# Performance work log

Hardware: AMD Instinct MI355X
Metric: run time of the kernel (lower is better)

Reference implementation:

```python
import jax, jax.numpy as jnp
import numpy as np

LN_EPS = 1e-5


def setup_inputs() -> dict:
    key = jax.random.key(0)
    ks = jax.random.split(key, 12)
    b, m, d = 4096, 64, 256
    s = 1.0 / np.sqrt(d)
    return {
        "head_left": jax.random.normal(ks[0], (b, d), jnp.float32),
        "rel_left": jax.random.normal(ks[1], (b, m, d), jnp.float32),
        "tail_left": jax.random.normal(ks[2], (b, m, d), jnp.float32),
        "head_right": jax.random.normal(ks[3], (b, d), jnp.float32),
        "rel_right": jax.random.normal(ks[4], (b, m, d), jnp.float32),
        "tail_right": jax.random.normal(ks[5], (b, m, d), jnp.float32),
        "mask_left": jax.random.randint(ks[6], (b, m), 0, 2).astype(bool),
        "mask_right": jax.random.randint(ks[7], (b, m), 0, 2).astype(bool),
        "bilinear_w": jax.random.normal(ks[8], (d, d), jnp.float32) * s,
        "w_tail": jax.random.normal(ks[9], (d, d), jnp.float32) * s,
        "w_head": jax.random.normal(ks[10], (d, d), jnp.float32) * s,
        "ln_gamma": jnp.ones((d,), jnp.float32),
        "ln_beta": jnp.zeros((d,), jnp.float32),
    }


def _intra_attention(weak_rel, rel, tail, mask, bilinear_w):
    # score[b,m] = weak_rel[b,:] @ W @ rel[b,m,:]  (nn.Bilinear with out=1, no bias)
    hW = weak_rel @ bilinear_w                      # [b, d]
    score = jnp.einsum("bd,bmd->bm", hW, rel)       # [b, m]
    score = jnp.where(mask, -jnp.inf, score)
    att = jax.nn.softmax(score, axis=1)             # [b, m]
    return jnp.einsum("bm,bmd->bd", att, tail)      # weighted sum of tails


def _layer_norm(x, gamma, beta):
    mu = jnp.mean(x, axis=-1, keepdims=True)
    var = jnp.var(x, axis=-1, keepdims=True)
    return (x - mu) * jax.lax.rsqrt(var + LN_EPS) * gamma + beta


def reference(head_left, rel_left, tail_left, head_right, rel_right, tail_right,
              mask_left, mask_right, bilinear_w, w_tail, w_head, ln_gamma, ln_beta):
    weak_rel = head_right - head_left
    left = _intra_attention(weak_rel, rel_left, tail_left, mask_left, bilinear_w)
    right = _intra_attention(weak_rel, rel_right, tail_right, mask_right, bilinear_w)
    # torch Linear: x @ W.T ; dropout p=0.0 is identity
    left = jax.nn.relu(left @ w_tail.T + head_left @ w_head.T)
    right = jax.nn.relu(right @ w_tail.T + head_right @ w_head.T)
    left = _layer_norm(left + head_left, ln_gamma, ln_beta)
    right = _layer_norm(right + head_right, ln_gamma, ln_beta)
    return (left, right)
```

## Files before the change

### kernel.cpp

```cpp
#include <hip/hip_runtime.h>

#define NB 4096
#define MM 64
#define DD 256
#define LN_EPS 1e-5f
#define NEG_BIG -1e30f

typedef float f4v __attribute__((ext_vector_type(4)));

#define WS_WCAT 0
#define WS_HW   (512 * DD)
#define WS_CTX  (WS_HW + NB * DD)

__global__ __launch_bounds__(256)
void k_prep(const float* __restrict__ head_left,
            const float* __restrict__ head_right,
            const float* __restrict__ bw,
            const float* __restrict__ wt,
            const float* __restrict__ wh,
            float* __restrict__ wcat,
            float* __restrict__ hW)
{
    __shared__ float smem[64 * 65];
    const int t = threadIdx.x;

    if (blockIdx.x < 32) {
        const int mat   = blockIdx.x >> 4;
        const int tile  = blockIdx.x & 15;
        const int dBase = (tile >> 2) * 64;
        const int kBase = (tile & 3) * 64;
        const float* __restrict__ w = mat ? wh : wt;
        float (*tile_s)[65] = (float(*)[65])smem;
        const int c  = t & 63;
        const int rr = t >> 6;
        #pragma unroll
        for (int r = rr; r < 64; r += 4)
            tile_s[r][c] = w[(dBase + r) * DD + kBase + c];
        __syncthreads();
        #pragma unroll
        for (int kr = rr; kr < 64; kr += 4)
            wcat[(mat * 256 + kBase + kr) * DD + dBase + c] = tile_s[c][kr];
    } else {
        const int blk  = blockIdx.x - 32;
        const int lane = t & 63;
        const int w    = t >> 6;
        float (*weak_s)[DD] = (float(*)[DD])smem;
        #pragma unroll
        for (int r = 0; r < 16; ++r) {
            const size_t idx = (size_t)(blk * 16 + r) * DD + t;
            weak_s[r][t] = head_right[idx] - head_left[idx];
        }
        __syncthreads();

        float4 acc[4];
        #pragma unroll
        for (int r = 0; r < 4; ++r) acc[r] = make_float4(0.f, 0.f, 0.f, 0.f);
        for (int k = 0; k < DD; ++k) {
            const float4 w4 = *(const float4*)(bw + k * DD + 4 * lane);
            #pragma unroll
            for (int r = 0; r < 4; ++r) {
                const float x = weak_s[4 * w + r][k];
                acc[r].x += x * w4.x; acc[r].y += x * w4.y;
                acc[r].z += x * w4.z; acc[r].w += x * w4.w;
            }
        }
        #pragma unroll
        for (int r = 0; r < 4; ++r)
            *(float4*)(hW + (size_t)(blk * 16 + 4 * w + r) * DD + 4 * lane) = acc[r];
    }
}

__global__ __launch_bounds__(256)
void k_attn(const float* __restrict__ rel_left,
            const float* __restrict__ tail_left,
            const float* __restrict__ rel_right,
            const float* __restrict__ tail_right,
            const unsigned char* __restrict__ mask_left,
            const unsigned char* __restrict__ mask_right,
            const float* __restrict__ hW,
            float* __restrict__ ctx)
{
    const int b    = blockIdx.x >> 1;
    const int side = blockIdx.x & 1;
    const int t    = threadIdx.x;
    const int lane = t & 63;
    const int w    = t >> 6;

    const float* __restrict__ rel  = side ? rel_right  : rel_left;
    const float* __restrict__ tail = side ? tail_right : tail_left;
    const unsigned char* __restrict__ mask = side ? mask_right : mask_left;

    __shared__ float part_s[MM][65];
    __shared__ float red_s[MM][5];
    __shared__ float att_s[MM];
    __shared__ float cpart_s[4][DD];

    const float4 hw4 = *(const float4*)(hW + (size_t)b * DD + 4 * lane);
    const float* rp = rel  + (size_t)b * MM * DD + 4 * lane;
    const float* tp = tail + (size_t)b * MM * DD + 4 * lane;

    #pragma unroll
    for (int i = 0; i < 16; ++i) {
        const int m = w * 16 + i;
        const f4v r4 = __builtin_nontemporal_load((const f4v*)(rp + (size_t)m * DD));
        part_s[m][lane] = hw4.x * r4.x + hw4.y * r4.y + hw4.z * r4.z + hw4.w * r4.w;
    }
    __syncthreads();

    {
        const int m = t & 63;
        const int c = t >> 6;
        float s = 0.f;
        #pragma unroll
        for (int j = 0; j < 16; ++j) s += part_s[m][c * 16 + j];
        red_s[m][c] = s;
    }
    __syncthreads();

    if (w == 0) {
        const unsigned char v0 = mask_left[lane];
        const bool mask_u8 = (__ballot(((lane & 3) != 0) && (v0 != 0)) != 0ULL);

        float s = red_s[lane][0] + red_s[lane][1] + red_s[lane][2] + red_s[lane][3];
        const bool msk = mask_u8
            ? (mask[(size_t)b * MM + lane] != 0)
            : (((const int*)(const void*)mask)[(size_t)b * MM + lane] != 0);
        if (msk) s = NEG_BIG;
        float mx = s;
        #pragma unroll
        for (int off = 32; off >= 1; off >>= 1) mx = fmaxf(mx, __shfl_xor(mx, off, 64));
        const float e = __expf(s - mx);
        float sum = e;
        #pragma unroll
        for (int off = 32; off >= 1; off >>= 1) sum += __shfl_xor(sum, off, 64);
        att_s[lane] = e / sum;
    }
    __syncthreads();

    float4 acc = make_float4(0.f, 0.f, 0.f, 0.f);
    #pragma unroll 4
    for (int i = 0; i < 16; ++i) {
        const int m = w * 16 + i;
        const float a  = att_s[m];
        const f4v v = __builtin_nontemporal_load((const f4v*)(tp + (size_t)m * DD));
        acc.x += a * v.x; acc.y += a * v.y; acc.z += a * v.z; acc.w += a * v.w;
    }
    *(float4*)(&cpart_s[w][4 * lane]) = acc;
    __syncthreads();

    const float sum = cpart_s[0][t] + cpart_s[1][t] + cpart_s[2][t] + cpart_s[3][t];
    ctx[(size_t)(side * NB + b) * DD + t] = sum;
}

__global__ __launch_bounds__(256)
void k_outln(const float* __restrict__ ctx,
             const float* __restrict__ head_left,
             const float* __restrict__ head_right,
             const float* __restrict__ wcat,
             const float* __restrict__ gamma,
             const float* __restrict__ beta,
             float* __restrict__ out)
{
    const int blk  = blockIdx.x;
    const int t    = threadIdx.x;
    const int lane = t & 63;
    const int w    = t >> 6;

    __shared__ float x_s[16][512];

    const int  side = (blk * 16) >> 12;
    const float* __restrict__ head = side ? head_right : head_left;

    #pragma unroll
    for (int i = 0; i < 32; ++i) {
        const int idx = i * 256 + t;
        const int r   = idx >> 9;
        const int c   = idx & 511;
        const int rg  = blk * 16 + r;
        const int bb  = rg & (NB - 1);
        x_s[r][c] = (c < DD) ? ctx[(size_t)rg * DD + c]
                             : head[(size_t)bb * DD + (c - DD)];
    }
    __syncthreads();

    float4 acc[4];
    #pragma unroll
    for (int r = 0; r < 4; ++r) acc[r] = make_float4(0.f, 0.f, 0.f, 0.f);

    #pragma unroll 4
    for (int k = 0; k < 512; ++k) {
        const float4 w4 = *(const float4*)(wcat + (size_t)k * DD + 4 * lane);
        #pragma unroll
        for (int r = 0; r < 4; ++r) {
            const float x = x_s[4 * w + r][k];
            acc[r].x += x * w4.x; acc[r].y += x * w4.y;
            acc[r].z += x * w4.z; acc[r].w += x * w4.w;
        }
    }

    const float4 g4 = *(const float4*)(gamma + 4 * lane);
    const float4 b4 = *(const float4*)(beta  + 4 * lane);

    #pragma unroll
    for (int r = 0; r < 4; ++r) {
        const int rl = 4 * w + r;
        const float4 h4 = *(const float4*)(&x_s[rl][DD + 4 * lane]);
        float4 y;
        y.x = fmaxf(acc[r].x, 0.f) + h4.x;
        y.y = fmaxf(acc[r].y, 0.f) + h4.y;
        y.z = fmaxf(acc[r].z, 0.f) + h4.z;
        y.w = fmaxf(acc[r].w, 0.f) + h4.w;

        float s1 = y.x + y.y + y.z + y.w;
        float s2 = y.x * y.x + y.y * y.y + y.z * y.z + y.w * y.w;
        #pragma unroll
        for (int off = 32; off >= 1; off >>= 1) {
            s1 += __shfl_xor(s1, off, 64);
            s2 += __shfl_xor(s2, off, 64);
        }
        const float mu   = s1 * (1.0f / DD);
        const float var  = s2 * (1.0f / DD) - mu * mu;
        const float rstd = rsqrtf(var + LN_EPS);

        float4 o;
        o.x = (y.x - mu) * rstd * g4.x + b4.x;
        o.y = (y.y - mu) * rstd * g4.y + b4.y;
        o.z = (y.z - mu) * rstd * g4.z + b4.z;
        o.w = (y.w - mu) * rstd * g4.w + b4.w;
        *(float4*)(out + (size_t)(blk * 16 + rl) * DD + 4 * lane) = o;
    }
}

extern "C" void kernel_launch(void* const* d_in, const int* in_sizes, int n_in,
                              void* d_out, int out_size, void* d_ws, size_t ws_size,
                              hipStream_t stream) {
    const float* head_left  = (const float*)d_in[0];
    const float* rel_left   = (const float*)d_in[1];
    const float* tail_left  = (const float*)d_in[2];
    const float* head_right = (const float*)d_in[3];
    const float* rel_right  = (const float*)d_in[4];
    const float* tail_right = (const float*)d_in[5];
    const unsigned char* mask_left  = (const unsigned char*)d_in[6];
    const unsigned char* mask_right = (const unsigned char*)d_in[7];
    const float* bw    = (const float*)d_in[8];
    const float* wt    = (const float*)d_in[9];
    const float* wh    = (const float*)d_in[10];
    const float* gamma = (const float*)d_in[11];
    const float* beta  = (const float*)d_in[12];
    float* out = (float*)d_out;

    float* ws   = (float*)d_ws;
    float* wcat = ws + WS_WCAT;
    float* hW   = ws + WS_HW;
    float* ctxb = ws + WS_CTX;

    k_prep <<<dim3(288),  dim3(256), 0, stream>>>(head_left, head_right, bw, wt, wh, wcat, hW);
    k_attn <<<dim3(8192), dim3(256), 0, stream>>>(rel_left, tail_left, rel_right, tail_right,
                                                  mask_left, mask_right, hW, ctxb);
    k_outln<<<dim3(512),  dim3(256), 0, stream>>>(ctxb, head_left, head_right, wcat,
                                                  gamma, beta, out);
}
```

Measured before the change: 249.8 us.

## Drop LDS staging in output GEMM; each wave computes 8 rows from global

The output projection and LayerNorm kernel no longer stages 16 rows of ctx and head into shared memory. Each wave now handles 8 rows and reads its activations straight from global memory through wave-uniform addresses, which should turn into scalar loads. The block count is halved, so every weight float4 load is reused across 8 rows instead of 4. Outputs are written with nontemporal stores. In exchange there are fewer blocks (256 on a large GPU), more accumulator registers per thread, and a dependence on scalar-cache reads of the activations.

```diff
diff --git a/kernel.cpp b/kernel.cpp
--- a/kernel.cpp
+++ b/kernel.cpp
@@ -166,35 +166,39 @@
     const int lane = t & 63;
     const int w    = t >> 6;
 
-    __shared__ float x_s[16][512];
-
-    const int  side = (blk * 16) >> 12;
+    const int rg0  = __builtin_amdgcn_readfirstlane(blk * 32 + w * 8);
+    const int side = rg0 >> 12;
+    const int bb0  = rg0 & (NB - 1);
     const float* __restrict__ head = side ? head_right : head_left;
 
+    float4 acc[8];
     #pragma unroll
-    for (int i = 0; i < 32; ++i) {
-        const int idx = i * 256 + t;
-        const int r   = idx >> 9;
-        const int c   = idx & 511;
-        const int rg  = blk * 16 + r;
-        const int bb  = rg & (NB - 1);
-        x_s[r][c] = (c < DD) ? ctx[(size_t)rg * DD + c]
-                             : head[(size_t)bb * DD + (c - DD)];
-    }
-    __syncthreads();
-
-    float4 acc[4];
-    #pragma unroll
-    for (int r = 0; r < 4; ++r) acc[r] = make_float4(0.f, 0.f, 0.f, 0.f);
-
-    #pragma unroll 4
-    for (int k = 0; k < 512; ++k) {
-        const float4 w4 = *(const float4*)(wcat + (size_t)k * DD + 4 * lane);
-        #pragma unroll
-        for (int r = 0; r < 4; ++r) {
-            const float x = x_s[4 * w + r][k];
-            acc[r].x += x * w4.x; acc[r].y += x * w4.y;
-            acc[r].z += x * w4.z; acc[r].w += x * w4.w;
+    for (int r = 0; r < 8; ++r) acc[r] = make_float4(0.f, 0.f, 0.f, 0.f);
+
+    {
+        const float* __restrict__ xr = ctx + (size_t)rg0 * DD;
+        #pragma unroll 4
+        for (int k = 0; k < 256; ++k) {
+            const float4 w4 = *(const float4*)(wcat + (size_t)k * DD + 4 * lane);
+            #pragma unroll
+            for (int r = 0; r < 8; ++r) {
+                const float x = xr[r * DD + k];
+                acc[r].x += x * w4.x; acc[r].y += x * w4.y;
+                acc[r].z += x * w4.z; acc[r].w += x * w4.w;
+            }
+        }
+    }
+    {
+        const float* __restrict__ xh = head + (size_t)bb0 * DD;
+        #pragma unroll 4
+        for (int k = 0; k < 256; ++k) {
+            const float4 w4 = *(const float4*)(wcat + (size_t)(256 + k) * DD + 4 * lane);
+            #pragma unroll
+            for (int r = 0; r < 8; ++r) {
+                const float x = xh[r * DD + k];
+                acc[r].x += x * w4.x; acc[r].y += x * w4.y;
+                acc[r].z += x * w4.z; acc[r].w += x * w4.w;
+            }
         }
     }
 
@@ -202,9 +206,10 @@
     const float4 b4 = *(const float4*)(beta  + 4 * lane);
 
     #pragma unroll
-    for (int r = 0; r < 4; ++r) {
-        const int rl = 4 * w + r;
-        const float4 h4 = *(const float4*)(&x_s[rl][DD + 4 * lane]);
+    for (int r = 0; r < 8; ++r) {
+        const int rg = rg0 + r;
+        const int bb = rg & (NB - 1);
+        const float4 h4 = *(const float4*)(head + (size_t)bb * DD + 4 * lane);
         float4 y;
         y.x = fmaxf(acc[r].x, 0.f) + h4.x;
         y.y = fmaxf(acc[r].y, 0.f) + h4.y;
@@ -222,12 +227,12 @@
         const float var  = s2 * (1.0f / DD) - mu * mu;
         const float rstd = rsqrtf(var + LN_EPS);
 
-        float4 o;
+        f4v o;
         o.x = (y.x - mu) * rstd * g4.x + b4.x;
         o.y = (y.y - mu) * rstd * g4.y + b4.y;
         o.z = (y.z - mu) * rstd * g4.z + b4.z;
         o.w = (y.w - mu) * rstd * g4.w + b4.w;
-        *(float4*)(out + (size_t)(blk * 16 + rl) * DD + 4 * lane) = o;
+        __builtin_nontemporal_store(o, (f4v*)(out + (size_t)rg * DD + 4 * lane));
     }
 }
 
@@ -257,6 +262,6 @@
     k_prep <<<dim3(288),  dim3(256), 0, stream>>>(head_left, head_right, bw, wt, wh, wcat, hW);
     k_attn <<<dim3(8192), dim3(256), 0, stream>>>(rel_left, tail_left, rel_right, tail_right,
                                                   mask_left, mask_right, hW, ctxb);
-    k_outln<<<dim3(512),  dim3(256), 0, stream>>>(ctxb, head_left, head_right, wcat,
+    k_outln<<<dim3(256),  dim3(256), 0, stream>>>(ctxb, head_left, head_right, wcat,
                                                   gamma, beta, out);
 }
```

Measured after the change: 254.1 us. About the same (+1.7%).
